# Optimization experiments

Hardware: AMD Instinct MI355X
Metric: run time of the kernel (lower is better)

Reference implementation:

```python
import jax, jax.numpy as jnp
import numpy as np

N_NODES, N_EDGES = 1600, 32000
C = 128            # sphere_channels
LMAX, MMAX = 6, 2
M0 = LMAX + 1      # number of m=0 coefficients (7)
N_SPH = (LMAX + 1) ** 2   # 49 full harmonics after inverse Wigner rotation
BASIS = 512        # distance expansion size
MAX_ELEM = 90
HID = 128
RESCALE = 23.395238876342773


def _build_to_m(lmax, mmax):
    # CoefficientMappingModule.to_m: permutation from l-primary to m-primary order
    m_c = []
    for l in range(lmax + 1):
        mm = min(mmax, l)
        m_c.extend(range(-mm, mm + 1))
    m_c = np.array(m_c)
    n = len(m_c)
    to_m = np.zeros((n, n), np.float32)
    off = 0
    for m in range(mmax + 1):
        idx_r = np.nonzero(m_c == m)[0]
        for o, i in enumerate(idx_r):
            to_m[o + off, i] = 1.0
        off += len(idx_r)
        if m > 0:
            idx_i = np.nonzero(m_c == -m)[0]
            for o, i in enumerate(idx_i):
                to_m[o + off, i] = 1.0
            off += len(idx_i)
    return to_m

_TO_M = _build_to_m(LMAX, MMAX)
N_ALL = _TO_M.shape[0]   # 29


def setup_inputs() -> dict:
    key = jax.random.key(0)
    ks = jax.random.split(key, 12)
    d_in = BASIS + 2 * HID   # 768 (distance basis + source/target atom embeddings)
    return {
        "atomic_numbers": jax.random.randint(ks[0], (N_NODES,), 0, MAX_ELEM),
        "edge_distance": jax.random.uniform(ks[1], (N_EDGES, BASIS), dtype=jnp.float32),
        "edge_index": jax.random.randint(ks[2], (2, N_EDGES), 0, N_NODES),
        "src_table": jax.random.uniform(ks[3], (MAX_ELEM, HID), minval=-0.001, maxval=0.001),
        "tgt_table": jax.random.uniform(ks[4], (MAX_ELEM, HID), minval=-0.001, maxval=0.001),
        "w1": jax.random.normal(ks[5], (d_in, HID)) / np.float32(np.sqrt(d_in)),
        "b1": jnp.zeros((HID,), jnp.float32),
        "g1": jnp.ones((HID,), jnp.float32),
        "be1": jnp.zeros((HID,), jnp.float32),
        "w2": jax.random.normal(ks[6], (HID, HID)) / np.float32(np.sqrt(HID)),
        "b2": jnp.zeros((HID,), jnp.float32),
        "g2": jnp.ones((HID,), jnp.float32),
        "be2": jnp.zeros((HID,), jnp.float32),
        "w3": jax.random.normal(ks[7], (HID, M0 * C)) / np.float32(np.sqrt(HID)),
        "b3": jnp.zeros((M0 * C,), jnp.float32),
        "to_m": jnp.asarray(_TO_M),
        "wigner_inv": jax.random.normal(ks[8], (N_EDGES, N_SPH, N_ALL)) * 0.2,
    }


def _ln(x, g, b, eps=1e-5):
    mu = jnp.mean(x, axis=-1, keepdims=True)
    var = jnp.var(x, axis=-1, keepdims=True)
    return (x - mu) * jax.lax.rsqrt(var + eps) * g + b


def reference(atomic_numbers, edge_distance, edge_index, src_table, tgt_table,
              w1, b1, g1, be1, w2, b2, g2, be2, w3, b3, to_m, wigner_inv):
    E = edge_distance.shape[0]
    # atom-edge embedding gathers
    src = src_table[atomic_numbers[edge_index[0]]]            # [E, HID]
    tgt = tgt_table[atomic_numbers[edge_index[1]]]            # [E, HID]
    x = jnp.concatenate([edge_distance, src, tgt], axis=1)    # [E, 768]
    # RadialFunction: Linear -> LN -> SiLU -> Linear -> LN -> SiLU -> Linear
    h = jax.nn.silu(_ln(x @ w1 + b1, g1, be1))
    h = jax.nn.silu(_ln(h @ w2 + b2, g2, be2))
    x0 = (h @ w3 + b3).reshape(E, M0, C)                      # m=0 coefficients
    # _l_primary: to_m.T @ emb. Padded rows (m != 0) are zero, so only the
    # first M0 rows of to_m contribute.
    x_l = jnp.einsum("emc,ml->elc", x0, to_m[:M0])            # [E, N_ALL, C]
    # _rotate_inv: per-edge inverse Wigner-D rotation to full harmonics
    x_rot = jnp.einsum("eij,ejc->eic", wigner_inv, x_l)       # [E, N_SPH, C]
    # _reduce_edge: scatter-add onto target nodes, then rescale
    out = jax.ops.segment_sum(x_rot, edge_index[1], num_segments=N_NODES)
    return out / RESCALE
```

## Files before the change

### kernel.cpp

```cpp
#include <hip/hip_runtime.h>
#include <hip/hip_bf16.h>

#define NE 32000
#define NNODES 1600
#define CCH 128
#define M0C 7
#define NSPH 49
#define NALLC 29
#define BASIS 512
#define DIN 768
#define HID 128
#define RESCALE_F 23.395238876342773f
#define CH 28
#define MAXCH (NE / CH + NNODES)

typedef __bf16 bf16x8 __attribute__((ext_vector_type(8)));
typedef __bf16 bf16x2 __attribute__((ext_vector_type(2)));
typedef float  f32x4  __attribute__((ext_vector_type(4)));

__device__ __forceinline__ unsigned short f_to_bf16(float f) {
    unsigned int u = __float_as_uint(f);
    unsigned int r = (u + 0x7FFFu + ((u >> 16) & 1u)) >> 16;
    return (unsigned short)r;
}
__device__ __forceinline__ float silu_f(float x) {
    return x / (1.0f + __expf(-x));
}

__global__ __launch_bounds__(256) void prepack_w(
    const float* __restrict__ w1, const float* __restrict__ w2, const float* __restrict__ w3,
    unsigned short* __restrict__ w1p,
    unsigned short* __restrict__ w2p,
    unsigned short* __restrict__ w3p)
{
    int idx = blockIdx.x * 256 + threadIdx.x;
    if (idx < 98304) {
        int kstep = idx >> 12;
        int ct    = (idx >> 9) & 7;
        int li    = idx & 511;
        int lane = li >> 3, j = li & 7;
        int m = lane & 15, quad = lane >> 4;
        int k = kstep * 32 + quad * 8 + j;
        int n = ct * 16 + m;
        w1p[idx] = f_to_bf16(w1[(size_t)k * 128 + n]);
    } else if (idx < 114688) {
        int j2 = idx - 98304;
        int kstep = j2 >> 12;
        int ct    = (j2 >> 9) & 7;
        int li    = j2 & 511;
        int lane = li >> 3, j = li & 7;
        int m = lane & 15, quad = lane >> 4;
        int k = kstep * 32 + quad * 8 + j;
        int n = ct * 16 + m;
        w2p[j2] = f_to_bf16(w2[(size_t)k * 128 + n]);
    } else if (idx < 229376) {
        int j3 = idx - 114688;
        int kstep = j3 / 28672;
        int r     = j3 - kstep * 28672;
        int o     = r >> 12;
        int ctile = (r >> 9) & 7;
        int li    = r & 511;
        int lane = li >> 3, j = li & 7;
        int m = lane & 15, quad = lane >> 4;
        int k = kstep * 32 + quad * 8 + j;
        int n = o * 128 + ctile * 16 + m;
        w3p[j3] = f_to_bf16(w3[(size_t)k * 896 + n]);
    }
}

__global__ __launch_bounds__(256) void gemm1_ln_mfma(
    const float* __restrict__ dist,
    const int* __restrict__ edge_index,
    const int* __restrict__ atomic_numbers,
    const float* __restrict__ src_table,
    const float* __restrict__ tgt_table,
    const unsigned short* __restrict__ w1p,
    const float* __restrict__ bias,
    const float* __restrict__ gam,
    const float* __restrict__ bet,
    unsigned short* __restrict__ Out)
{
    const int t = threadIdx.x;
    const int wv = t >> 6, lane = t & 63;
    const int m = lane & 15, quad = lane >> 4;
    const int row0 = blockIdx.x * 64 + wv * 16;
    const int row = row0 + m;

    const int sid  = atomic_numbers[edge_index[row]];
    const int tid2 = atomic_numbers[edge_index[NE + row]];
    const float* a0 = dist + (size_t)row * 512 + quad * 8;
    const float* a1 = src_table + sid * 128 + quad * 8;
    const float* a2 = tgt_table + tid2 * 128 + quad * 8;
    const unsigned short* bb = w1p + lane * 8;

    f32x4 acc[8] = {};

#pragma unroll
    for (int k0 = 0; k0 < 768; k0 += 32) {
        const float* ap = (k0 < 512) ? (a0 + k0)
                        : (k0 < 640) ? (a1 + (k0 - 512))
                                     : (a2 + (k0 - 640));
        float4 va = *(const float4*)ap;
        float4 vb = *(const float4*)(ap + 4);
        bf16x8 af;
        af[0] = (__bf16)va.x; af[1] = (__bf16)va.y;
        af[2] = (__bf16)va.z; af[3] = (__bf16)va.w;
        af[4] = (__bf16)vb.x; af[5] = (__bf16)vb.y;
        af[6] = (__bf16)vb.z; af[7] = (__bf16)vb.w;
#pragma unroll
        for (int ct = 0; ct < 8; ++ct) {
            bf16x8 bfv = *(const bf16x8*)(bb + (size_t)(((k0 >> 5) * 8 + ct)) * 512);
            acc[ct] = __builtin_amdgcn_mfma_f32_16x16x32_bf16(af, bfv, acc[ct], 0, 0, 0);
        }
    }

    float bbv[8], ggv[8], eev[8];
#pragma unroll
    for (int ct = 0; ct < 8; ++ct) {
        bbv[ct] = bias[ct * 16 + m];
        ggv[ct] = gam[ct * 16 + m];
        eev[ct] = bet[ct * 16 + m];
    }
#pragma unroll
    for (int reg = 0; reg < 4; ++reg) {
        float v[8];
        float s = 0.f, s2 = 0.f;
#pragma unroll
        for (int ct = 0; ct < 8; ++ct) {
            v[ct] = acc[ct][reg] + bbv[ct];
            s += v[ct]; s2 += v[ct] * v[ct];
        }
#pragma unroll
        for (int off = 1; off < 16; off <<= 1) {
            s  += __shfl_xor(s, off, 64);
            s2 += __shfl_xor(s2, off, 64);
        }
        float mean = s * (1.0f / 128.0f);
        float var  = s2 * (1.0f / 128.0f) - mean * mean;
        float rstd = rsqrtf(var + 1e-5f);
        int orow = row0 + 4 * quad + reg;
#pragma unroll
        for (int ct = 0; ct < 8; ++ct) {
            float o = silu_f((v[ct] - mean) * rstd * ggv[ct] + eev[ct]);
            Out[(size_t)orow * 128 + ct * 16 + m] = f_to_bf16(o);
        }
    }
}

__global__ __launch_bounds__(256) void gemm2_ln_mfma(
    const unsigned short* __restrict__ A,
    const unsigned short* __restrict__ w2p,
    const float* __restrict__ bias,
    const float* __restrict__ gam,
    const float* __restrict__ bet,
    unsigned short* __restrict__ Out)
{
    const int t = threadIdx.x;
    const int wv = t >> 6, lane = t & 63;
    const int m = lane & 15, quad = lane >> 4;
    const int row0 = blockIdx.x * 64 + wv * 16;

    f32x4 acc[8] = {};
    const unsigned short* arow = A + (size_t)(row0 + m) * 128 + quad * 8;
    const unsigned short* bb   = w2p + lane * 8;

#pragma unroll
    for (int k0 = 0; k0 < 128; k0 += 32) {
        bf16x8 af = *(const bf16x8*)(arow + k0);
#pragma unroll
        for (int ct = 0; ct < 8; ++ct) {
            bf16x8 bfv = *(const bf16x8*)(bb + (size_t)(((k0 >> 5) * 8 + ct)) * 512);
            acc[ct] = __builtin_amdgcn_mfma_f32_16x16x32_bf16(af, bfv, acc[ct], 0, 0, 0);
        }
    }

    float bbv[8], ggv[8], eev[8];
#pragma unroll
    for (int ct = 0; ct < 8; ++ct) {
        bbv[ct] = bias[ct * 16 + m];
        ggv[ct] = gam[ct * 16 + m];
        eev[ct] = bet[ct * 16 + m];
    }
#pragma unroll
    for (int reg = 0; reg < 4; ++reg) {
        float v[8];
        float s = 0.f, s2 = 0.f;
#pragma unroll
        for (int ct = 0; ct < 8; ++ct) {
            v[ct] = acc[ct][reg] + bbv[ct];
            s += v[ct]; s2 += v[ct] * v[ct];
        }
#pragma unroll
        for (int off = 1; off < 16; off <<= 1) {
            s  += __shfl_xor(s, off, 64);
            s2 += __shfl_xor(s2, off, 64);
        }
        float mean = s * (1.0f / 128.0f);
        float var  = s2 * (1.0f / 128.0f) - mean * mean;
        float rstd = rsqrtf(var + 1e-5f);
        int row = row0 + 4 * quad + reg;
#pragma unroll
        for (int ct = 0; ct < 8; ++ct) {
            float o = silu_f((v[ct] - mean) * rstd * ggv[ct] + eev[ct]);
            Out[(size_t)row * 128 + ct * 16 + m] = f_to_bf16(o);
        }
    }
}

__global__ __launch_bounds__(256) void gemm3_mfma(
    const unsigned short* __restrict__ A,
    const unsigned short* __restrict__ w3p,
    const float* __restrict__ b3,
    unsigned short* __restrict__ X0p)
{
    const int t = threadIdx.x;
    const int wv = t >> 6, lane = t & 63;
    const int m = lane & 15, quad = lane >> 4;
    const int row0 = blockIdx.x * 16;
    const int c0 = wv * 32;

    f32x4 acc[14] = {};
    const unsigned short* arow = A + (size_t)(row0 + m) * 128 + quad * 8;
    const unsigned short* bb   = w3p + lane * 8;

#pragma unroll
    for (int k0 = 0; k0 < 128; k0 += 32) {
        bf16x8 af = *(const bf16x8*)(arow + k0);
#pragma unroll
        for (int o = 0; o < 7; ++o) {
#pragma unroll
            for (int ch2 = 0; ch2 < 2; ++ch2) {
                bf16x8 bfv = *(const bf16x8*)(bb +
                    (size_t)((((k0 >> 5) * 7 + o) * 8 + (wv * 2 + ch2))) * 512);
                acc[o * 2 + ch2] =
                    __builtin_amdgcn_mfma_f32_16x16x32_bf16(af, bfv, acc[o * 2 + ch2], 0, 0, 0);
            }
        }
    }

    const float inv_res = 1.0f / RESCALE_F;
    float bv[14];
#pragma unroll
    for (int o = 0; o < 7; ++o)
#pragma unroll
        for (int ch2 = 0; ch2 < 2; ++ch2)
            bv[o * 2 + ch2] = b3[o * 128 + c0 + ch2 * 16 + m];

#pragma unroll
    for (int reg = 0; reg < 4; ++reg) {
        int row = row0 + 4 * quad + reg;
#pragma unroll
        for (int ch2 = 0; ch2 < 2; ++ch2) {
            int c = c0 + ch2 * 16 + m;
            union { unsigned short us[8]; uint4 q; } pk;
#pragma unroll
            for (int o = 0; o < 7; ++o)
                pk.us[o] = f_to_bf16((acc[o * 2 + ch2][reg] + bv[o * 2 + ch2]) * inv_res);
            pk.us[7] = 0;
            *(uint4*)(X0p + (size_t)row * 1024 + c * 8) = pk.q;
        }
    }
}

__global__ __launch_bounds__(256) void hist_kernel(
    const int* __restrict__ edge_index, int* __restrict__ cnt)
{
    int e = blockIdx.x * 256 + threadIdx.x;
    if (e < NE) atomicAdd(&cnt[edge_index[NE + e]], 1);
}

__global__ __launch_bounds__(256) void scan_kernel(
    const int* __restrict__ cnt, int* __restrict__ offs, int* __restrict__ cur)
{
    __shared__ int part[256];
    const int t = threadIdx.x;
    const int base = t * 7;
    int s = 0;
#pragma unroll
    for (int j = 0; j < 7; ++j) {
        int i = base + j;
        if (i < NNODES) s += cnt[i];
    }
    part[t] = s;
    __syncthreads();
    for (int off = 1; off < 256; off <<= 1) {
        int v = (t >= off) ? part[t - off] : 0;
        __syncthreads();
        part[t] += v;
        __syncthreads();
    }
    int run = (t > 0) ? part[t - 1] : 0;
#pragma unroll
    for (int j = 0; j < 7; ++j) {
        int i = base + j;
        if (i < NNODES) {
            offs[i] = run;
            cur[i] = run;
            run += cnt[i];
        }
    }
    if (t == 0) offs[NNODES] = part[255];
}

__global__ __launch_bounds__(256) void scatter_kernel(
    const int* __restrict__ edge_index, int* __restrict__ cur, int* __restrict__ order)
{
    int e = blockIdx.x * 256 + threadIdx.x;
    if (e < NE) {
        int tgt = edge_index[NE + e];
        int pos = atomicAdd(&cur[tgt], 1);
        order[pos] = e;
    }
}

__global__ __launch_bounds__(256) void build_chunks(
    const int* __restrict__ offs, int* __restrict__ chunk_cnt,
    int* __restrict__ ch_node, int* __restrict__ ch_beg, int* __restrict__ ch_lm)
{
    int n = blockIdx.x * 256 + threadIdx.x;
    if (n >= NNODES) return;
    int b = offs[n], k = offs[n + 1] - b;
    if (k == 0) return;
    int nc = (k + CH - 1) / CH;
    int base = atomicAdd(chunk_cnt, nc);
    for (int c = 0; c < nc; ++c) {
        ch_node[base + c] = n;
        ch_beg[base + c]  = b + CH * c;
        int l = min(CH, k - CH * c);
        ch_lm[base + c] = l | ((nc > 1) ? 0x10000 : 0);
    }
}

__global__ __launch_bounds__(256) void rotate_chunks_mfma(
    const unsigned short* __restrict__ X0p,
    const float* __restrict__ wig,
    const int* __restrict__ order,
    const int* __restrict__ chunk_cnt,
    const int* __restrict__ ch_node,
    const int* __restrict__ ch_beg,
    const int* __restrict__ ch_lm,
    float* __restrict__ out)
{
    __shared__ unsigned short Ws[CH][64][8];
    __shared__ int es[CH];

    const int b = blockIdx.x;
    if (b >= chunk_cnt[0]) return;
    const int node = ch_node[b];
    const int beg  = ch_beg[b];
    const int lm   = ch_lm[b];
    const int len  = lm & 0xFFFF;
    const int multi = lm >> 16;

    const int t = threadIdx.x;
    const int wv = t >> 6, lane = t & 63;
    const int m = lane & 15, quad = lane >> 4;

    if (t < CH) es[t] = order[beg + ((t < len) ? t : 0)];

    const int slot8 = t >> 3;
    const int lane8 = t & 7;
    if (slot8 < CH) {
        const int e = (slot8 < len) ? order[beg + slot8] : -1;
        const float* wsrc = wig + (size_t)e * (NSPH * NALLC);
#pragma unroll
        for (int j = 0; j < 49; ++j) {
            int idx = j * 8 + lane8;
            int i = idx >> 3, o = idx & 7;
            float v = 0.f;
            if (e >= 0 && o < 7) {
                int col = (o < 2) ? (2 * o) : (5 * o - 4);
                v = wsrc[i * NALLC + col];
            }
            Ws[slot8][i][o] = f_to_bf16(v);
        }
#pragma unroll
        for (int j = 0; j < 15; ++j)
            Ws[slot8][49 + j][lane8] = 0;
    }
    __syncthreads();

    f32x4 acc[8] = {};
    for (int g = 0; g < 7; ++g) {
        const int e = es[g * 4 + quad];
        const unsigned short* xb = X0p + (size_t)e * 1024 + m * 8;
        bf16x8 aq = *(const bf16x8*)&Ws[g * 4 + quad][wv * 16 + m][0];
#pragma unroll
        for (int nt = 0; nt < 8; ++nt) {
            bf16x8 bq = *(const bf16x8*)(xb + nt * 128);
            acc[nt] = __builtin_amdgcn_mfma_f32_16x16x32_bf16(aq, bq, acc[nt], 0, 0, 0);
        }
    }

    float* op = out + (size_t)node * (NSPH * CCH);
    const int r0 = wv * 16 + quad * 4;
    if (multi) {
#pragma unroll
        for (int nt = 0; nt < 8; ++nt) {
            int c = nt * 16 + m;
#pragma unroll
            for (int reg = 0; reg < 4; ++reg) {
                int sph = r0 + reg;
                if (sph < NSPH) atomicAdd(&op[sph * CCH + c], acc[nt][reg]);
            }
        }
    } else {
#pragma unroll
        for (int nt = 0; nt < 8; ++nt) {
            int c = nt * 16 + m;
#pragma unroll
            for (int reg = 0; reg < 4; ++reg) {
                int sph = r0 + reg;
                if (sph < NSPH) op[sph * CCH + c] = acc[nt][reg];
            }
        }
    }
}

extern "C" void kernel_launch(void* const* d_in, const int* in_sizes, int n_in,
                              void* d_out, int out_size, void* d_ws, size_t ws_size,
                              hipStream_t stream) {
    const int*   atomic_numbers = (const int*)d_in[0];
    const float* edge_distance  = (const float*)d_in[1];
    const int*   edge_index     = (const int*)d_in[2];
    const float* src_table      = (const float*)d_in[3];
    const float* tgt_table      = (const float*)d_in[4];
    const float* w1  = (const float*)d_in[5];
    const float* b1  = (const float*)d_in[6];
    const float* g1  = (const float*)d_in[7];
    const float* be1 = (const float*)d_in[8];
    const float* w2  = (const float*)d_in[9];
    const float* b2  = (const float*)d_in[10];
    const float* g2  = (const float*)d_in[11];
    const float* be2 = (const float*)d_in[12];
    const float* w3  = (const float*)d_in[13];
    const float* b3  = (const float*)d_in[14];
    const float* wig = (const float*)d_in[16];

    char* ws = (char*)d_ws;
    unsigned short* H1b = (unsigned short*)(ws);
    unsigned short* H2b = (unsigned short*)(ws + 8192000);
    unsigned short* X0p = (unsigned short*)(ws + 16384000);
    unsigned short* w1p = (unsigned short*)(ws + 81920000);
    unsigned short* w2p = (unsigned short*)(ws + 82116608);
    unsigned short* w3p = (unsigned short*)(ws + 82149376);
    int* ints      = (int*)(ws + 82378752);
    int* cnt       = ints;
    int* chunk_cnt = cnt + NNODES;
    int* offs      = chunk_cnt + 1;
    int* cur       = offs + NNODES + 1;
    int* order     = cur + NNODES;
    int* ch_node   = order + NE;
    int* ch_beg    = ch_node + MAXCH;
    int* ch_lm     = ch_beg + MAXCH;

    hipMemsetAsync(cnt, 0, (NNODES + 1) * sizeof(int), stream);
    hipMemsetAsync(d_out, 0, (size_t)out_size * sizeof(float), stream);

    hist_kernel<<<(NE + 255) / 256, 256, 0, stream>>>(edge_index, cnt);
    scan_kernel<<<1, 256, 0, stream>>>(cnt, offs, cur);
    scatter_kernel<<<(NE + 255) / 256, 256, 0, stream>>>(edge_index, cur, order);
    build_chunks<<<(NNODES + 255) / 256, 256, 0, stream>>>(
        offs, chunk_cnt, ch_node, ch_beg, ch_lm);

    prepack_w<<<(229376 + 255) / 256, 256, 0, stream>>>(w1, w2, w3, w1p, w2p, w3p);
    gemm1_ln_mfma<<<NE / 64, 256, 0, stream>>>(
        edge_distance, edge_index, atomic_numbers, src_table, tgt_table,
        w1p, b1, g1, be1, H1b);
    gemm2_ln_mfma<<<NE / 64, 256, 0, stream>>>(H1b, w2p, b2, g2, be2, H2b);
    gemm3_mfma<<<NE / 16, 256, 0, stream>>>(H2b, w3p, b3, X0p);

    rotate_chunks_mfma<<<MAXCH, 256, 0, stream>>>(
        X0p, wig, order, chunk_cnt, ch_node, ch_beg, ch_lm, (float*)d_out);
}
```

Before: 453.6 us.

## Stage edge_distance tile in LDS for gemm1 and pre-extract Wigner columns

```diff
diff --git a/kernel.cpp b/kernel.cpp
--- a/kernel.cpp
+++ b/kernel.cpp
@@ -13,6 +13,10 @@
 #define RESCALE_F 23.395238876342773f
 #define CH 28
 #define MAXCH (NE / CH + NNODES)
+#define WCROW 8
+#define WCPE (NSPH * WCROW)
+#define WC_OFF 82558976ull
+#define WC_BYTES (2ull * NE * WCPE)
 
 typedef __bf16 bf16x8 __attribute__((ext_vector_type(8)));
 typedef __bf16 bf16x2 __attribute__((ext_vector_type(2)));
@@ -80,33 +84,54 @@
     const float* __restrict__ bet,
     unsigned short* __restrict__ Out)
 {
+    __shared__ unsigned short Ad[64][512];
+
     const int t = threadIdx.x;
     const int wv = t >> 6, lane = t & 63;
     const int m = lane & 15, quad = lane >> 4;
-    const int row0 = blockIdx.x * 64 + wv * 16;
-    const int row = row0 + m;
-
+    const int row0 = blockIdx.x * 64;
+
+    {
+        const float4* src = (const float4*)(dist + (size_t)row0 * 512);
+#pragma unroll 8
+        for (int it = 0; it < 32; ++it) {
+            int u = it * 256 + t;
+            float4 v = src[u];
+            int row = u >> 7;
+            int c4  = (u & 127) * 4;
+            int gs  = (c4 >> 3) ^ (row & 7);
+            unsigned short* d = &Ad[row][gs * 8 + (c4 & 7)];
+            d[0] = f_to_bf16(v.x); d[1] = f_to_bf16(v.y);
+            d[2] = f_to_bf16(v.z); d[3] = f_to_bf16(v.w);
+        }
+    }
+
+    const int arow = wv * 16 + m;
+    const int row  = row0 + arow;
     const int sid  = atomic_numbers[edge_index[row]];
     const int tid2 = atomic_numbers[edge_index[NE + row]];
-    const float* a0 = dist + (size_t)row * 512 + quad * 8;
     const float* a1 = src_table + sid * 128 + quad * 8;
     const float* a2 = tgt_table + tid2 * 128 + quad * 8;
     const unsigned short* bb = w1p + lane * 8;
+    __syncthreads();
 
     f32x4 acc[8] = {};
 
 #pragma unroll
     for (int k0 = 0; k0 < 768; k0 += 32) {
-        const float* ap = (k0 < 512) ? (a0 + k0)
-                        : (k0 < 640) ? (a1 + (k0 - 512))
-                                     : (a2 + (k0 - 640));
-        float4 va = *(const float4*)ap;
-        float4 vb = *(const float4*)(ap + 4);
         bf16x8 af;
-        af[0] = (__bf16)va.x; af[1] = (__bf16)va.y;
-        af[2] = (__bf16)va.z; af[3] = (__bf16)va.w;
-        af[4] = (__bf16)vb.x; af[5] = (__bf16)vb.y;
-        af[6] = (__bf16)vb.z; af[7] = (__bf16)vb.w;
+        if (k0 < 512) {
+            int gs = ((k0 >> 3) + quad) ^ (arow & 7);
+            af = *(const bf16x8*)&Ad[arow][gs * 8];
+        } else {
+            const float* ap = (k0 < 640) ? (a1 + (k0 - 512)) : (a2 + (k0 - 640));
+            float4 va = *(const float4*)ap;
+            float4 vb = *(const float4*)(ap + 4);
+            af[0] = (__bf16)va.x; af[1] = (__bf16)va.y;
+            af[2] = (__bf16)va.z; af[3] = (__bf16)va.w;
+            af[4] = (__bf16)vb.x; af[5] = (__bf16)vb.y;
+            af[6] = (__bf16)vb.z; af[7] = (__bf16)vb.w;
+        }
 #pragma unroll
         for (int ct = 0; ct < 8; ++ct) {
             bf16x8 bfv = *(const bf16x8*)(bb + (size_t)(((k0 >> 5) * 8 + ct)) * 512);
@@ -138,7 +163,7 @@
         float mean = s * (1.0f / 128.0f);
         float var  = s2 * (1.0f / 128.0f) - mean * mean;
         float rstd = rsqrtf(var + 1e-5f);
-        int orow = row0 + 4 * quad + reg;
+        int orow = row0 + wv * 16 + 4 * quad + reg;
 #pragma unroll
         for (int ct = 0; ct < 8; ++ct) {
             float o = silu_f((v[ct] - mean) * rstd * ggv[ct] + eev[ct]);
@@ -331,9 +356,53 @@
     }
 }
 
+__global__ __launch_bounds__(256) void wig_extract(
+    const float* __restrict__ wig,
+    const int* __restrict__ order,
+    unsigned short* __restrict__ Wc)
+{
+    __shared__ float raw[8 * 1421];
+    __shared__ int eloc[8];
+
+    const int t = threadIdx.x;
+    const int p0 = blockIdx.x * 8;
+    if (t < 8) eloc[t] = order[p0 + t];
+    __syncthreads();
+
+    {
+        const int g = t >> 5, l = t & 31;
+        const float* src = wig + (size_t)eloc[g] * (NSPH * NALLC);
+        float* dst = raw + g * 1421;
+#pragma unroll
+        for (int it = 0; it < 45; ++it) {
+            int i = it * 32 + l;
+            if (i < 1421) dst[i] = src[i];
+        }
+    }
+    __syncthreads();
+
+    uint4* wout = (uint4*)(Wc + (size_t)p0 * WCPE);
+    for (int q = t; q < 8 * NSPH; q += 256) {
+        int pl = q / NSPH, row = q - pl * NSPH;
+        const float* r = raw + pl * 1421 + row * NALLC;
+        union { unsigned short us[8]; uint4 v; } pk;
+        pk.us[0] = f_to_bf16(r[0]);
+        pk.us[1] = f_to_bf16(r[2]);
+        pk.us[2] = f_to_bf16(r[6]);
+        pk.us[3] = f_to_bf16(r[11]);
+        pk.us[4] = f_to_bf16(r[16]);
+        pk.us[5] = f_to_bf16(r[21]);
+        pk.us[6] = f_to_bf16(r[26]);
+        pk.us[7] = 0;
+        wout[q] = pk.v;
+    }
+}
+
 __global__ __launch_bounds__(256) void rotate_chunks_mfma(
     const unsigned short* __restrict__ X0p,
     const float* __restrict__ wig,
+    const unsigned short* __restrict__ Wc,
+    const int use_wc,
     const int* __restrict__ order,
     const int* __restrict__ chunk_cnt,
     const int* __restrict__ ch_node,
@@ -358,25 +427,40 @@
 
     if (t < CH) es[t] = order[beg + ((t < len) ? t : 0)];
 
-    const int slot8 = t >> 3;
-    const int lane8 = t & 7;
-    if (slot8 < CH) {
-        const int e = (slot8 < len) ? order[beg + slot8] : -1;
-        const float* wsrc = wig + (size_t)e * (NSPH * NALLC);
-#pragma unroll
-        for (int j = 0; j < 49; ++j) {
-            int idx = j * 8 + lane8;
-            int i = idx >> 3, o = idx & 7;
-            float v = 0.f;
-            if (e >= 0 && o < 7) {
-                int col = (o < 2) ? (2 * o) : (5 * o - 4);
-                v = wsrc[i * NALLC + col];
+    if (use_wc) {
+        const uint4* wsrc = (const uint4*)(Wc + (size_t)beg * WCPE);
+        const int nval = len * NSPH;
+        for (int q = t; q < CH * NSPH; q += 256) {
+            int slot = q / NSPH, row = q - slot * NSPH;
+            uint4 v = make_uint4(0u, 0u, 0u, 0u);
+            if (q < nval) v = wsrc[q];
+            *(uint4*)&Ws[slot][row][0] = v;
+        }
+        for (int q = t; q < CH * 15; q += 256) {
+            int slot = q / 15, row = 49 + (q - (q / 15) * 15);
+            *(uint4*)&Ws[slot][row][0] = make_uint4(0u, 0u, 0u, 0u);
+        }
+    } else {
+        const int slot8 = t >> 3;
+        const int lane8 = t & 7;
+        if (slot8 < CH) {
+            const int e = (slot8 < len) ? order[beg + slot8] : -1;
+            const float* wsrc = wig + (size_t)e * (NSPH * NALLC);
+#pragma unroll
+            for (int j = 0; j < 49; ++j) {
+                int idx = j * 8 + lane8;
+                int i = idx >> 3, o = idx & 7;
+                float v = 0.f;
+                if (e >= 0 && o < 7) {
+                    int col = (o < 2) ? (2 * o) : (5 * o - 4);
+                    v = wsrc[i * NALLC + col];
+                }
+                Ws[slot8][i][o] = f_to_bf16(v);
             }
-            Ws[slot8][i][o] = f_to_bf16(v);
-        }
-#pragma unroll
-        for (int j = 0; j < 15; ++j)
-            Ws[slot8][49 + j][lane8] = 0;
+#pragma unroll
+            for (int j = 0; j < 15; ++j)
+                Ws[slot8][49 + j][lane8] = 0;
+        }
     }
     __syncthreads();
 
@@ -453,6 +537,8 @@
     int* ch_node   = order + NE;
     int* ch_beg    = ch_node + MAXCH;
     int* ch_lm     = ch_beg + MAXCH;
+    const int use_wc = (ws_size >= WC_OFF + WC_BYTES) ? 1 : 0;
+    unsigned short* Wc = (unsigned short*)(ws + WC_OFF);
 
     hipMemsetAsync(cnt, 0, (NNODES + 1) * sizeof(int), stream);
     hipMemsetAsync(d_out, 0, (size_t)out_size * sizeof(float), stream);
@@ -462,6 +548,9 @@
     scatter_kernel<<<(NE + 255) / 256, 256, 0, stream>>>(edge_index, cur, order);
     build_chunks<<<(NNODES + 255) / 256, 256, 0, stream>>>(
         offs, chunk_cnt, ch_node, ch_beg, ch_lm);
+
+    if (use_wc)
+        wig_extract<<<NE / 8, 256, 0, stream>>>(wig, order, Wc);
 
     prepack_w<<<(229376 + 255) / 256, 256, 0, stream>>>(w1, w2, w3, w1p, w2p, w3p);
     gemm1_ln_mfma<<<NE / 64, 256, 0, stream>>>(
@@ -471,5 +560,6 @@
     gemm3_mfma<<<NE / 16, 256, 0, stream>>>(H2b, w3p, b3, X0p);
 
     rotate_chunks_mfma<<<MAXCH, 256, 0, stream>>>(
-        X0p, wig, order, chunk_cnt, ch_node, ch_beg, ch_lm, (float*)d_out);
-}
+        X0p, wig, Wc, use_wc, order, chunk_cnt, ch_node, ch_beg, ch_lm,
+        (float*)d_out);
+}
```

After: 465.1 us. +2.5%, slower.
